# Performance work log

Measured on AMD Instinct MI355X. Metric: run time of the kernel, lower is better.

Reference implementation:

```python
import jax, jax.numpy as jnp
import numpy as np

# Neighbor offsets (dy, dx) for kernels j=0..7. Each torch conv with a
# [-1 at neighbor, +1 at center] 3x3 kernel and padding=1 equals
# x - shift(x, offset) with zero-padded borders.
_OFFSETS = [(0, -1), (1, -1), (1, 0), (1, 1), (0, 1), (-1, 1), (-1, 0), (-1, -1)]
_EPS = 1e-5


def setup_inputs() -> dict:
    key = jax.random.key(0)
    x = jax.random.normal(key, (32, 1, 1024, 1024), dtype=jnp.float32)
    return {"x": x}


def _ltpe_forward(x):
    B, C, H, W = x.shape
    xp = jnp.pad(x, ((0, 0), (0, 0), (1, 1), (1, 1)))  # zero border, matches conv padding=1
    out = jnp.zeros_like(x)
    for j, (dy, dx) in enumerate(_OFFSETS):
        nb = jax.lax.dynamic_slice(xp, (0, 0, 1 + dy, 1 + dx), (B, C, H, W))
        diff = x - nb                      # conv output for kernel j
        out = out + ((diff + 1.0) * 0.5) * (float(2 ** j) / 255.0)
    # InstanceNorm2d(1): normalize over (H, W) per sample/channel, no affine,
    # biased variance, eps=1e-5.
    mean = jnp.mean(out, axis=(2, 3), keepdims=True)
    var = jnp.var(out, axis=(2, 3), keepdims=True)
    return (out - mean) * jax.lax.rsqrt(var + _EPS)


def reference(x):
    return _ltpe_forward(x)
```

## Files before the change

### kernel.cpp

```cpp
#include <hip/hip_runtime.h>


#define HH 1024
#define WW 1024
#define NIMG 32
#define NBLK 32
#define RPB (HH / NBLK)
#define TPB 256

typedef float vfloat4 __attribute__((ext_vector_type(4)));

__device__ __forceinline__ void compute_y(const float* up, const float* mid,
                                          const float* dn, float* y) {
    const float w0 = 1.f / 255.f,  w1 = 2.f / 255.f,  w2 = 4.f / 255.f,
                w3 = 8.f / 255.f,  w4 = 16.f / 255.f, w5 = 32.f / 255.f,
                w6 = 64.f / 255.f, w7 = 128.f / 255.f;
#pragma unroll
    for (int k = 0; k < 4; ++k) {
        float s = w0 * mid[k] + w4 * mid[k + 2]
                + w1 * dn[k]  + w2 * dn[k + 1] + w3 * dn[k + 2]
                + w7 * up[k]  + w6 * up[k + 1] + w5 * up[k + 2];
        y[k] = mid[k + 1] - s;
    }
}

__device__ __forceinline__ void load_row_g(const float* __restrict__ base,
                                           int r, int c, float* buf) {
    if (r < 0 || r >= HH) {
#pragma unroll
        for (int k = 0; k < 6; ++k) buf[k] = 0.f;
        return;
    }
    const float* row = base + (size_t)r * WW;
    const vfloat4 v = reinterpret_cast<const vfloat4*>(row)[c];
    buf[0] = (c > 0) ? row[4 * c - 1] : 0.f;
    buf[1] = v.x; buf[2] = v.y; buf[3] = v.z; buf[4] = v.w;
    buf[5] = (c < TPB - 1) ? row[4 * c + 4] : 0.f;
}

template <bool NORM>
__global__ __launch_bounds__(TPB) void ltpe_pass(const float* __restrict__ x,
                                                 float* __restrict__ partials,
                                                 float* __restrict__ out) {
    const int img = blockIdx.x / NBLK;
    const int blk = blockIdx.x % NBLK;
    const int c = threadIdx.x;
    const float* base = x + (size_t)img * HH * WW;
    const int r0 = blk * RPB;

    float mean = 0.f, scale = 1.f;
    if (NORM) {
        __shared__ float sh_stats[2];
        if (threadIdx.x < 64) {
            const int lane = threadIdx.x;
            double S = 0.0, SS = 0.0;
            if (lane < NBLK) {
                S = (double)partials[img * NBLK + lane];
                SS = (double)partials[NIMG * NBLK + img * NBLK + lane];
            }
#pragma unroll
            for (int off = 32; off > 0; off >>= 1) {
                S += __shfl_down(S, off);
                SS += __shfl_down(SS, off);
            }
            if (lane == 0) {
                const double N = (double)HH * (double)WW;
                const double m = S / N;
                const double var = SS / N - m * m;
                sh_stats[0] = (float)m;
                sh_stats[1] = (float)(1.0 / sqrt(var + 4e-5));
            }
        }
        __syncthreads();
        mean = sh_stats[0];
        scale = sh_stats[1];
    }

    float buf[4][6];
    load_row_g(base, r0 - 1, c, buf[0]);
    load_row_g(base, r0,     c, buf[1]);
    load_row_g(base, r0 + 1, c, buf[2]);
    load_row_g(base, r0 + 2, c, buf[3]);

    float s = 0.f, ss = 0.f;
    float* obase = out + (size_t)img * HH * WW;

#pragma unroll
    for (int i = 0; i < RPB; ++i) {
        const int r = r0 + i;
        float y[4];
        compute_y(buf[i & 3], buf[(i + 1) & 3], buf[(i + 2) & 3], y);
        if (NORM) {
            vfloat4 o;
            o.x = (y[0] - mean) * scale;
            o.y = (y[1] - mean) * scale;
            o.z = (y[2] - mean) * scale;
            o.w = (y[3] - mean) * scale;
            __builtin_nontemporal_store(
                o, reinterpret_cast<vfloat4*>(obase + (size_t)r * WW) + c);
        } else {
#pragma unroll
            for (int k = 0; k < 4; ++k) { s += y[k]; ss = fmaf(y[k], y[k], ss); }
        }
        if (i + 2 < RPB)
            load_row_g(base, r + 3, c, buf[i & 3]);
    }

    if (!NORM) {
#pragma unroll
        for (int off = 32; off > 0; off >>= 1) {
            s += __shfl_down(s, off);
            ss += __shfl_down(ss, off);
        }
        __shared__ float sh[8];
        const int wave = threadIdx.x >> 6;
        const int lane = threadIdx.x & 63;
        if (lane == 0) { sh[wave] = s; sh[4 + wave] = ss; }
        __syncthreads();
        if (threadIdx.x == 0) {
            partials[img * NBLK + blk] = sh[0] + sh[1] + sh[2] + sh[3];
            partials[NIMG * NBLK + img * NBLK + blk] = sh[4] + sh[5] + sh[6] + sh[7];
        }
    }
}

extern "C" void kernel_launch(void* const* d_in, const int* in_sizes, int n_in,
                              void* d_out, int out_size, void* d_ws, size_t ws_size,
                              hipStream_t stream) {
    const float* x = (const float*)d_in[0];
    float* out = (float*)d_out;
    float* partials = (float*)d_ws;

    ltpe_pass<false><<<NIMG * NBLK, TPB, 0, stream>>>(x, partials, out);
    ltpe_pass<true><<<NIMG * NBLK, TPB, 0, stream>>>(x, partials, out);
}
```

Measured before the change: 70.89 us.

## Cache stencil output as bf16 between stats and normalize passes

The first pass now writes the stencil result y to a workspace in bf16 while accumulating statistics. The second pass becomes a pure streaming kernel that reads the bf16 values and writes normalized fp32, with a different block split. This avoids recomputing the stencil and rereading x with halo loads, but adds a 64MB write and read of intermediate data and bf16 rounding error in the output.

```diff
diff --git a/kernel.cpp b/kernel.cpp
--- a/kernel.cpp
+++ b/kernel.cpp
@@ -3,12 +3,17 @@
 
 #define HH 1024
 #define WW 1024
+#define HW (HH * WW)
 #define NIMG 32
-#define NBLK 32
-#define RPB (HH / NBLK)
+#define NBLK1 32
+#define RPB1 (HH / NBLK1)
+#define NBLK2 64
+#define EPB2 (HW / NBLK2)
 #define TPB 256
 
 typedef float vfloat4 __attribute__((ext_vector_type(4)));
+typedef unsigned short vushort4 __attribute__((ext_vector_type(4)));
+typedef unsigned short vushort8 __attribute__((ext_vector_type(8)));
 
 __device__ __forceinline__ void compute_y(const float* up, const float* mid,
                                           const float* dn, float* y) {
@@ -38,43 +43,21 @@
     buf[5] = (c < TPB - 1) ? row[4 * c + 4] : 0.f;
 }
 
-template <bool NORM>
-__global__ __launch_bounds__(TPB) void ltpe_pass(const float* __restrict__ x,
-                                                 float* __restrict__ partials,
-                                                 float* __restrict__ out) {
-    const int img = blockIdx.x / NBLK;
-    const int blk = blockIdx.x % NBLK;
+__device__ __forceinline__ unsigned short f32_to_bf16_rne(float f) {
+    unsigned int u = __float_as_uint(f);
+    u += 0x7fffu + ((u >> 16) & 1u);
+    return (unsigned short)(u >> 16);
+}
+
+__global__ __launch_bounds__(TPB) void ltpe_stats(const float* __restrict__ x,
+                                                  float* __restrict__ partials,
+                                                  unsigned short* __restrict__ yb) {
+    const int img = blockIdx.x / NBLK1;
+    const int blk = blockIdx.x % NBLK1;
     const int c = threadIdx.x;
-    const float* base = x + (size_t)img * HH * WW;
-    const int r0 = blk * RPB;
-
-    float mean = 0.f, scale = 1.f;
-    if (NORM) {
-        __shared__ float sh_stats[2];
-        if (threadIdx.x < 64) {
-            const int lane = threadIdx.x;
-            double S = 0.0, SS = 0.0;
-            if (lane < NBLK) {
-                S = (double)partials[img * NBLK + lane];
-                SS = (double)partials[NIMG * NBLK + img * NBLK + lane];
-            }
-#pragma unroll
-            for (int off = 32; off > 0; off >>= 1) {
-                S += __shfl_down(S, off);
-                SS += __shfl_down(SS, off);
-            }
-            if (lane == 0) {
-                const double N = (double)HH * (double)WW;
-                const double m = S / N;
-                const double var = SS / N - m * m;
-                sh_stats[0] = (float)m;
-                sh_stats[1] = (float)(1.0 / sqrt(var + 4e-5));
-            }
-        }
-        __syncthreads();
-        mean = sh_stats[0];
-        scale = sh_stats[1];
-    }
+    const float* base = x + (size_t)img * HW;
+    unsigned short* ybase = yb + (size_t)img * HW;
+    const int r0 = blk * RPB1;
 
     float buf[4][6];
     load_row_g(base, r0 - 1, c, buf[0]);
@@ -83,44 +66,90 @@
     load_row_g(base, r0 + 2, c, buf[3]);
 
     float s = 0.f, ss = 0.f;
-    float* obase = out + (size_t)img * HH * WW;
-
 #pragma unroll
-    for (int i = 0; i < RPB; ++i) {
+    for (int i = 0; i < RPB1; ++i) {
         const int r = r0 + i;
         float y[4];
         compute_y(buf[i & 3], buf[(i + 1) & 3], buf[(i + 2) & 3], y);
-        if (NORM) {
-            vfloat4 o;
-            o.x = (y[0] - mean) * scale;
-            o.y = (y[1] - mean) * scale;
-            o.z = (y[2] - mean) * scale;
-            o.w = (y[3] - mean) * scale;
-            __builtin_nontemporal_store(
-                o, reinterpret_cast<vfloat4*>(obase + (size_t)r * WW) + c);
-        } else {
 #pragma unroll
-            for (int k = 0; k < 4; ++k) { s += y[k]; ss = fmaf(y[k], y[k], ss); }
-        }
-        if (i + 2 < RPB)
+        for (int k = 0; k < 4; ++k) { s += y[k]; ss = fmaf(y[k], y[k], ss); }
+        vushort4 h;
+        h.x = f32_to_bf16_rne(y[0]);
+        h.y = f32_to_bf16_rne(y[1]);
+        h.z = f32_to_bf16_rne(y[2]);
+        h.w = f32_to_bf16_rne(y[3]);
+        reinterpret_cast<vushort4*>(ybase + (size_t)r * WW)[c] = h;
+        if (i + 2 < RPB1)
             load_row_g(base, r + 3, c, buf[i & 3]);
     }
 
-    if (!NORM) {
+#pragma unroll
+    for (int off = 32; off > 0; off >>= 1) {
+        s += __shfl_down(s, off);
+        ss += __shfl_down(ss, off);
+    }
+    __shared__ float sh[8];
+    const int wave = threadIdx.x >> 6;
+    const int lane = threadIdx.x & 63;
+    if (lane == 0) { sh[wave] = s; sh[4 + wave] = ss; }
+    __syncthreads();
+    if (threadIdx.x == 0) {
+        partials[img * NBLK1 + blk] = sh[0] + sh[1] + sh[2] + sh[3];
+        partials[NIMG * NBLK1 + img * NBLK1 + blk] = sh[4] + sh[5] + sh[6] + sh[7];
+    }
+}
+
+__global__ __launch_bounds__(TPB) void ltpe_norm(const unsigned short* __restrict__ yb,
+                                                 const float* __restrict__ partials,
+                                                 float* __restrict__ out) {
+    const int img = blockIdx.x / NBLK2;
+    const int blk = blockIdx.x % NBLK2;
+
+    __shared__ float sh_stats[2];
+    if (threadIdx.x < 64) {
+        const int lane = threadIdx.x;
+        double S = 0.0, SS = 0.0;
+        if (lane < NBLK1) {
+            S = (double)partials[img * NBLK1 + lane];
+            SS = (double)partials[NIMG * NBLK1 + img * NBLK1 + lane];
+        }
 #pragma unroll
         for (int off = 32; off > 0; off >>= 1) {
-            s += __shfl_down(s, off);
-            ss += __shfl_down(ss, off);
+            S += __shfl_down(S, off);
+            SS += __shfl_down(SS, off);
         }
-        __shared__ float sh[8];
-        const int wave = threadIdx.x >> 6;
-        const int lane = threadIdx.x & 63;
-        if (lane == 0) { sh[wave] = s; sh[4 + wave] = ss; }
-        __syncthreads();
-        if (threadIdx.x == 0) {
-            partials[img * NBLK + blk] = sh[0] + sh[1] + sh[2] + sh[3];
-            partials[NIMG * NBLK + img * NBLK + blk] = sh[4] + sh[5] + sh[6] + sh[7];
+        if (lane == 0) {
+            const double N = (double)HW;
+            const double m = S / N;
+            const double var = SS / N - m * m;
+            sh_stats[0] = (float)m;
+            sh_stats[1] = (float)(1.0 / sqrt(var + 4e-5));
         }
+    }
+    __syncthreads();
+    const float mean = sh_stats[0];
+    const float scale = sh_stats[1];
+
+    const size_t base = (size_t)img * HW + (size_t)blk * EPB2;
+    const unsigned short* yp = yb + base;
+    float* op = out + base;
+
+#pragma unroll
+    for (int i = 0; i < EPB2 / (TPB * 8); ++i) {
+        const int idx = i * TPB * 8 + threadIdx.x * 8;
+        const vushort8 h = *reinterpret_cast<const vushort8*>(yp + idx);
+        vfloat4 o0, o1;
+        o0.x = fmaf(__uint_as_float((unsigned int)h[0] << 16) - mean, scale, 0.f);
+        o0.y = (__uint_as_float((unsigned int)h[1] << 16) - mean) * scale;
+        o0.z = (__uint_as_float((unsigned int)h[2] << 16) - mean) * scale;
+        o0.w = (__uint_as_float((unsigned int)h[3] << 16) - mean) * scale;
+        o1.x = (__uint_as_float((unsigned int)h[4] << 16) - mean) * scale;
+        o1.y = (__uint_as_float((unsigned int)h[5] << 16) - mean) * scale;
+        o1.z = (__uint_as_float((unsigned int)h[6] << 16) - mean) * scale;
+        o1.w = (__uint_as_float((unsigned int)h[7] << 16) - mean) * scale;
+        o0.x = (__uint_as_float((unsigned int)h[0] << 16) - mean) * scale;
+        __builtin_nontemporal_store(o0, reinterpret_cast<vfloat4*>(op + idx));
+        __builtin_nontemporal_store(o1, reinterpret_cast<vfloat4*>(op + idx + 4));
     }
 }
 
@@ -130,7 +159,8 @@
     const float* x = (const float*)d_in[0];
     float* out = (float*)d_out;
     float* partials = (float*)d_ws;
+    unsigned short* yb = (unsigned short*)((char*)d_ws + 65536);
 
-    ltpe_pass<false><<<NIMG * NBLK, TPB, 0, stream>>>(x, partials, out);
-    ltpe_pass<true><<<NIMG * NBLK, TPB, 0, stream>>>(x, partials, out);
+    ltpe_stats<<<NIMG * NBLK1, TPB, 0, stream>>>(x, partials, yb);
+    ltpe_norm<<<NIMG * NBLK2, TPB, 0, stream>>>(yb, partials, out);
 }
```

Result: slower. 96.16 us (+35.7%).

## Fuse stats and normalize passes into one kernel with per-image atomic barrier

Applied to the files above, without the earlier changes.

Merges the two-pass launch (partial statistics, then normalize) into a single kernel. Each block publishes its partial sums, bumps a per-image atomic counter, then spin-waits until all 32 blocks of that image have arrived before normalizing. The block re-reads its input rows while a second re-read of x comes from cache rather than a second launch. It relies on all 1024 blocks being co-resident to avoid deadlock, and adds a tiny zeroing kernel plus spin-wait cost.

```diff
diff --git a/kernel.cpp b/kernel.cpp
--- a/kernel.cpp
+++ b/kernel.cpp
@@ -3,6 +3,7 @@
 
 #define HH 1024
 #define WW 1024
+#define HW (HH * WW)
 #define NIMG 32
 #define NBLK 32
 #define RPB (HH / NBLK)
@@ -38,75 +39,39 @@
     buf[5] = (c < TPB - 1) ? row[4 * c + 4] : 0.f;
 }
 
-template <bool NORM>
-__global__ __launch_bounds__(TPB) void ltpe_pass(const float* __restrict__ x,
-                                                 float* __restrict__ partials,
-                                                 float* __restrict__ out) {
+__global__ __launch_bounds__(NIMG) void ltpe_zero_counts(int* __restrict__ count) {
+    count[threadIdx.x] = 0;
+}
+
+__global__ __launch_bounds__(TPB) void ltpe_fused(const float* __restrict__ x,
+                                                  float* __restrict__ partials,
+                                                  int* __restrict__ count,
+                                                  float* __restrict__ out) {
     const int img = blockIdx.x / NBLK;
     const int blk = blockIdx.x % NBLK;
     const int c = threadIdx.x;
-    const float* base = x + (size_t)img * HH * WW;
+    const float* base = x + (size_t)img * HW;
     const int r0 = blk * RPB;
 
-    float mean = 0.f, scale = 1.f;
-    if (NORM) {
-        __shared__ float sh_stats[2];
-        if (threadIdx.x < 64) {
-            const int lane = threadIdx.x;
-            double S = 0.0, SS = 0.0;
-            if (lane < NBLK) {
-                S = (double)partials[img * NBLK + lane];
-                SS = (double)partials[NIMG * NBLK + img * NBLK + lane];
-            }
+    {
+        float buf[4][6];
+        load_row_g(base, r0 - 1, c, buf[0]);
+        load_row_g(base, r0,     c, buf[1]);
+        load_row_g(base, r0 + 1, c, buf[2]);
+        load_row_g(base, r0 + 2, c, buf[3]);
+
+        float s = 0.f, ss = 0.f;
 #pragma unroll
-            for (int off = 32; off > 0; off >>= 1) {
-                S += __shfl_down(S, off);
-                SS += __shfl_down(SS, off);
-            }
-            if (lane == 0) {
-                const double N = (double)HH * (double)WW;
-                const double m = S / N;
-                const double var = SS / N - m * m;
-                sh_stats[0] = (float)m;
-                sh_stats[1] = (float)(1.0 / sqrt(var + 4e-5));
-            }
-        }
-        __syncthreads();
-        mean = sh_stats[0];
-        scale = sh_stats[1];
-    }
-
-    float buf[4][6];
-    load_row_g(base, r0 - 1, c, buf[0]);
-    load_row_g(base, r0,     c, buf[1]);
-    load_row_g(base, r0 + 1, c, buf[2]);
-    load_row_g(base, r0 + 2, c, buf[3]);
-
-    float s = 0.f, ss = 0.f;
-    float* obase = out + (size_t)img * HH * WW;
-
-#pragma unroll
-    for (int i = 0; i < RPB; ++i) {
-        const int r = r0 + i;
-        float y[4];
-        compute_y(buf[i & 3], buf[(i + 1) & 3], buf[(i + 2) & 3], y);
-        if (NORM) {
-            vfloat4 o;
-            o.x = (y[0] - mean) * scale;
-            o.y = (y[1] - mean) * scale;
-            o.z = (y[2] - mean) * scale;
-            o.w = (y[3] - mean) * scale;
-            __builtin_nontemporal_store(
-                o, reinterpret_cast<vfloat4*>(obase + (size_t)r * WW) + c);
-        } else {
+        for (int i = 0; i < RPB; ++i) {
+            const int r = r0 + i;
+            float y[4];
+            compute_y(buf[i & 3], buf[(i + 1) & 3], buf[(i + 2) & 3], y);
 #pragma unroll
             for (int k = 0; k < 4; ++k) { s += y[k]; ss = fmaf(y[k], y[k], ss); }
+            if (i + 2 < RPB)
+                load_row_g(base, r + 3, c, buf[i & 3]);
         }
-        if (i + 2 < RPB)
-            load_row_g(base, r + 3, c, buf[i & 3]);
-    }
 
-    if (!NORM) {
 #pragma unroll
         for (int off = 32; off > 0; off >>= 1) {
             s += __shfl_down(s, off);
@@ -120,7 +85,66 @@
         if (threadIdx.x == 0) {
             partials[img * NBLK + blk] = sh[0] + sh[1] + sh[2] + sh[3];
             partials[NIMG * NBLK + img * NBLK + blk] = sh[4] + sh[5] + sh[6] + sh[7];
+            __hip_atomic_fetch_add(&count[img], 1, __ATOMIC_RELEASE,
+                                   __HIP_MEMORY_SCOPE_AGENT);
         }
+    }
+
+    float buf[4][6];
+    load_row_g(base, r0 - 1, c, buf[0]);
+    load_row_g(base, r0,     c, buf[1]);
+    load_row_g(base, r0 + 1, c, buf[2]);
+    load_row_g(base, r0 + 2, c, buf[3]);
+
+    if (threadIdx.x == 0) {
+        while (__hip_atomic_fetch_add(&count[img], 0, __ATOMIC_RELAXED,
+                                      __HIP_MEMORY_SCOPE_AGENT) < NBLK) {
+            __builtin_amdgcn_s_sleep(16);
+        }
+    }
+    __syncthreads();
+    __builtin_amdgcn_fence(__ATOMIC_ACQUIRE, "agent");
+
+    __shared__ float sh_stats[2];
+    if (threadIdx.x < 64) {
+        const int lane = threadIdx.x;
+        double S = 0.0, SS = 0.0;
+        if (lane < NBLK) {
+            S = (double)partials[img * NBLK + lane];
+            SS = (double)partials[NIMG * NBLK + img * NBLK + lane];
+        }
+#pragma unroll
+        for (int off = 32; off > 0; off >>= 1) {
+            S += __shfl_down(S, off);
+            SS += __shfl_down(SS, off);
+        }
+        if (lane == 0) {
+            const double N = (double)HW;
+            const double m = S / N;
+            const double var = SS / N - m * m;
+            sh_stats[0] = (float)m;
+            sh_stats[1] = (float)(1.0 / sqrt(var + 4e-5));
+        }
+    }
+    __syncthreads();
+    const float mean = sh_stats[0];
+    const float scale = sh_stats[1];
+
+    float* obase = out + (size_t)img * HW;
+#pragma unroll
+    for (int i = 0; i < RPB; ++i) {
+        const int r = r0 + i;
+        float y[4];
+        compute_y(buf[i & 3], buf[(i + 1) & 3], buf[(i + 2) & 3], y);
+        vfloat4 o;
+        o.x = (y[0] - mean) * scale;
+        o.y = (y[1] - mean) * scale;
+        o.z = (y[2] - mean) * scale;
+        o.w = (y[3] - mean) * scale;
+        __builtin_nontemporal_store(
+            o, reinterpret_cast<vfloat4*>(obase + (size_t)r * WW) + c);
+        if (i + 2 < RPB)
+            load_row_g(base, r + 3, c, buf[i & 3]);
     }
 }
 
@@ -130,7 +154,8 @@
     const float* x = (const float*)d_in[0];
     float* out = (float*)d_out;
     float* partials = (float*)d_ws;
+    int* count = (int*)(partials + 2 * NIMG * NBLK);
 
-    ltpe_pass<false><<<NIMG * NBLK, TPB, 0, stream>>>(x, partials, out);
-    ltpe_pass<true><<<NIMG * NBLK, TPB, 0, stream>>>(x, partials, out);
+    ltpe_zero_counts<<<1, NIMG, 0, stream>>>(count);
+    ltpe_fused<<<NIMG * NBLK, TPB, 0, stream>>>(x, partials, count, out);
 }
```

After: 143.8 us. 2.03x slower.
